# Kernel tuning notes

Hardware: AMD Instinct MI355X
Metric: run time of the kernel (lower is better)

Reference implementation:

```python
import jax, jax.numpy as jnp
import numpy as np

N_LABELS = 24
LABEL_DIM = 256
NEG = -10000.0


def setup_inputs() -> dict:
    key = jax.random.key(0)
    k1, k2 = jax.random.split(key, 2)
    B, L, DIM = 8, 512, 1024
    features = jax.random.normal(k1, (B, L, DIM), dtype=jnp.float32)
    mask = jnp.ones((B, L), dtype=bool)
    w_ff = jax.random.normal(k2, (N_LABELS * LABEL_DIM * 2, DIM), dtype=jnp.float32) * 0.02
    b_ff = jnp.zeros((N_LABELS * LABEL_DIM * 2,), dtype=jnp.float32)
    bias = jnp.zeros((N_LABELS,), dtype=jnp.float32)
    return {"features": features, "mask": mask, "w_ff": w_ff, "b_ff": b_ff, "bias": bias}


def reference(features, mask, w_ff, b_ff, bias):
    B, L, _ = features.shape
    # ff -> relu -> split into start/end features per label
    x = jax.nn.relu(jnp.einsum('bld,od->blo', features, w_ff) + b_ff)  # [B,L,n_labels*label_dim*2]
    x = x.reshape(B, L, N_LABELS, LABEL_DIM, 2)
    start_f = x[..., 0]  # [B,L,n_labels,label_dim]
    end_f = x[..., 1]
    # biaffine pairwise span scores: [B, n_labels, start, end]
    scores = jnp.einsum('bsld,beld->blse', start_f, end_f) + bias[None, :, None, None]
    # remove_nan branch: replace inf/nan with -10000
    scores = jnp.where(jnp.isinf(scores) | jnp.isnan(scores), NEG, scores)
    # triangular + padding mask over (start, end)
    triu = jnp.triu(jnp.ones((L, L), dtype=bool))  # start <= end
    spans_mask = triu[None] & mask[:, :, None] & mask[:, None, :]  # [B,L,L]
    masked_scores = jnp.where(spans_mask[:, None, :, :], scores, NEG)
    return scores, masked_scores
```

## Files before the change

### kernel.cpp

```cpp
#include <hip/hip_runtime.h>
#include <hip/hip_bf16.h>

#define NLAB  24
#define LDIM  256
#define LSEQ  512
#define DDIM  1024
#define NOUT  12288
#define NEGV  (-10000.0f)
#define MOFF  50331648L

typedef __attribute__((ext_vector_type(8))) short short8;
typedef __attribute__((ext_vector_type(4))) float f32x4;
typedef unsigned short u16;
typedef unsigned int   u32;

typedef const __attribute__((address_space(1))) void gvoid_t;
typedef __attribute__((address_space(3))) void lvoid_t;

__device__ __forceinline__ u16 f2bf(float f) {
  u32 u = __builtin_bit_cast(u32, f);
  u32 r = u + 0x7FFFu + ((u >> 16) & 1u);
  return (u16)(r >> 16);
}

__device__ __forceinline__ void g2l16(const u16* g, u16* l) {
  __builtin_amdgcn_global_load_lds((gvoid_t*)g, (lvoid_t*)l, 16, 0, 0);
}

__global__ void cvt_bf16_kernel(const float* __restrict__ feat,
                                const float* __restrict__ wff,
                                u16* __restrict__ fA, u16* __restrict__ fB) {
  const long NA = 4194304L;
  const long NB = 12582912L;
  const long NQ = (NA + NB) / 4;
  long stride = (long)gridDim.x * blockDim.x;
  for (long i = (long)blockIdx.x * blockDim.x + threadIdx.x; i < NQ; i += stride) {
    long e = i * 4;
    const float* s; u16* d;
    if (e < NA) { s = feat + e;        d = fA + e; }
    else        { s = wff + (e - NA);  d = fB + (e - NA); }
    float4 v = *reinterpret_cast<const float4*>(s);
    ushort4 o;
    o.x = f2bf(v.x); o.y = f2bf(v.y); o.z = f2bf(v.z); o.w = f2bf(v.w);
    *reinterpret_cast<ushort4*>(d) = o;
  }
}

template<int LDK, bool PERM>
__device__ __forceinline__ void stage_tile(const u16* __restrict__ gbase, int row0,
                                           int k0, u16* lbuf, int t) {
#pragma unroll
  for (int l = 0; l < 4; ++l) {
    const int rt = l * 64 + (t >> 3);
    const int ce = ((t & 7) ^ (rt & 7)) << 3;
    int gr = rt;
    if (PERM) gr = (rt & ~31) | ((rt & 15) << 1) | ((rt >> 4) & 1);
    g2l16(gbase + (long)(row0 + gr) * LDK + k0 + ce, lbuf + (l * 512 + t) * 8);
  }
}

#define FRAG_OFF(r, ks, hi) (((r) * 64 + (ks) * 32 + (hi) * 8) ^ (((r) & 7) << 3))

__global__ __launch_bounds__(512, 2)
void ff_gemm256(const u16* __restrict__ A, const u16* __restrict__ B,
                const float* __restrict__ bff,
                u16* __restrict__ sf, u16* __restrict__ ef) {
  __shared__ __align__(16) u16 lds[2][2][16384];
  const int tid = threadIdx.x, lane = tid & 63, wv = tid >> 6;
  const int wm = wv >> 2, wn = wv & 3;
  const int lr = lane & 15, hi = lane >> 4;

  const int bid = blockIdx.x;
  const int wg  = (bid & 7) * 96 + (bid >> 3);
  const int tm  = wg & 15, tn = wg >> 4;
  const int rowA0 = tm * 256, rowB0 = tn * 256;

  f32x4 acc[8][4] = {};

  stage_tile<DDIM, false>(A, rowA0, 0, lds[0][0], tid);
  stage_tile<DDIM, true >(B, rowB0, 0, lds[0][1], tid);
  __syncthreads();

  int buf = 0;
  for (int t = 0; t < 16; ++t) {
    if (t < 15) {
      stage_tile<DDIM, false>(A, rowA0, (t + 1) * 64, lds[buf ^ 1][0], tid);
      stage_tile<DDIM, true >(B, rowB0, (t + 1) * 64, lds[buf ^ 1][1], tid);
    }
    const u16* La = lds[buf][0];
    const u16* Lb = lds[buf][1];
#pragma unroll
    for (int ks = 0; ks < 2; ++ks) {
      short8 af[8], bfr[4];
#pragma unroll
      for (int i = 0; i < 8; ++i) {
        const int r = wm * 128 + i * 16 + lr;
        af[i] = *reinterpret_cast<const short8*>(La + FRAG_OFF(r, ks, hi));
      }
#pragma unroll
      for (int j = 0; j < 4; ++j) {
        const int r = wn * 64 + j * 16 + lr;
        bfr[j] = *reinterpret_cast<const short8*>(Lb + FRAG_OFF(r, ks, hi));
      }
      __builtin_amdgcn_s_setprio(1);
#pragma unroll
      for (int i = 0; i < 8; ++i)
#pragma unroll
        for (int j = 0; j < 4; ++j)
          acc[i][j] = __builtin_amdgcn_mfma_f32_16x16x32_bf16(af[i], bfr[j], acc[i][j], 0, 0, 0);
      __builtin_amdgcn_s_setprio(0);
    }
    __syncthreads();
    buf ^= 1;
  }

#pragma unroll
  for (int j = 0; j < 4; ++j) {
    const int cblk = wn * 64 + j * 16;
    const int o = rowB0 + (cblk & ~31) + 2 * lr + ((cblk >> 4) & 1);
    const float bv = bff[o];
    const int label = o >> 9, d = (o >> 1) & 255, se = o & 1;
    u16* dst = se ? ef : sf;
#pragma unroll
    for (int i = 0; i < 8; ++i) {
#pragma unroll
      for (int r = 0; r < 4; ++r) {
        const int m = rowA0 + wm * 128 + i * 16 + hi * 4 + r;
        const int b = m >> 9, ll = m & 511;
        float v = acc[i][j][r] + bv;
        v = v > 0.f ? v : 0.f;
        dst[((long)(b * NLAB + label) * LSEQ + ll) * LDIM + d] = f2bf(v);
      }
    }
  }
}

__global__ __launch_bounds__(512, 2)
void biaffine256(const u16* __restrict__ sf, const u16* __restrict__ ef,
                 const float* __restrict__ bias, const int* __restrict__ mask,
                 float* __restrict__ out) {
  __shared__ __align__(16) u16 lds[2][2][16384];
  const int tid = threadIdx.x, lane = tid & 63, wv = tid >> 6;
  const int wm = wv >> 2, wn = wv & 3;
  const int lr = lane & 15, hi = lane >> 4;

  const int bid = blockIdx.x;
  const int wg  = (bid & 7) * 96 + (bid >> 3);
  const int bl  = wg >> 2, tile = wg & 3;
  const int tm  = tile >> 1, tn = tile & 1;
  const int b = bl / NLAB, label = bl - b * NLAB;
  const u16* Ab = sf + (long)bl * LSEQ * LDIM;
  const u16* Bb = ef + (long)bl * LSEQ * LDIM;
  const int rowA0 = tm * 256, rowB0 = tn * 256;

  f32x4 acc[8][4] = {};

  stage_tile<LDIM, false>(Ab, rowA0, 0, lds[0][0], tid);
  stage_tile<LDIM, false>(Bb, rowB0, 0, lds[0][1], tid);
  __syncthreads();

  int buf = 0;
  for (int t = 0; t < 4; ++t) {
    if (t < 3) {
      stage_tile<LDIM, false>(Ab, rowA0, (t + 1) * 64, lds[buf ^ 1][0], tid);
      stage_tile<LDIM, false>(Bb, rowB0, (t + 1) * 64, lds[buf ^ 1][1], tid);
    }
    const u16* La = lds[buf][0];
    const u16* Lb = lds[buf][1];
#pragma unroll
    for (int ks = 0; ks < 2; ++ks) {
      short8 af[8], bfr[4];
#pragma unroll
      for (int i = 0; i < 8; ++i) {
        const int r = wm * 128 + i * 16 + lr;
        af[i] = *reinterpret_cast<const short8*>(La + FRAG_OFF(r, ks, hi));
      }
#pragma unroll
      for (int j = 0; j < 4; ++j) {
        const int r = wn * 64 + j * 16 + lr;
        bfr[j] = *reinterpret_cast<const short8*>(Lb + FRAG_OFF(r, ks, hi));
      }
      __builtin_amdgcn_s_setprio(1);
#pragma unroll
      for (int i = 0; i < 8; ++i)
#pragma unroll
        for (int j = 0; j < 4; ++j)
          acc[i][j] = __builtin_amdgcn_mfma_f32_16x16x32_bf16(af[i], bfr[j], acc[i][j], 0, 0, 0);
      __builtin_amdgcn_s_setprio(0);
    }
    __syncthreads();
    buf ^= 1;
  }

  const float bv = bias[label];
  const long obase = (long)bl * LSEQ * LSEQ;
#pragma unroll
  for (int i = 0; i < 8; ++i) {
#pragma unroll
    for (int r = 0; r < 4; ++r) {
      const int s = rowA0 + wm * 128 + i * 16 + hi * 4 + r;
      const bool ms = (mask[b * LSEQ + s] != 0);
      const long rbase = obase + (long)s * LSEQ;
#pragma unroll
      for (int j = 0; j < 4; ++j) {
        const int e = rowB0 + wn * 64 + j * 16 + lr;
        float v = acc[i][j][r] + bv;
        u32 bits = __builtin_bit_cast(u32, v);
        if ((bits & 0x7F800000u) == 0x7F800000u) v = NEGV;
        out[rbase + e] = v;
        const bool keep = (s <= e) && ms && (mask[b * LSEQ + e] != 0);
        out[MOFF + rbase + e] = keep ? v : NEGV;
      }
    }
  }
}

extern "C" void kernel_launch(void* const* d_in, const int* in_sizes, int n_in,
                              void* d_out, int out_size, void* d_ws, size_t ws_size,
                              hipStream_t stream) {
  const float* feat = (const float*)d_in[0];
  const int*   mask = (const int*)d_in[1];
  const float* wff  = (const float*)d_in[2];
  const float* bff  = (const float*)d_in[3];
  const float* bias = (const float*)d_in[4];
  float* out = (float*)d_out;

  u16* fA = (u16*)d_ws;
  u16* fB = fA + 4194304L;
  u16* sf = fB + 12582912L;
  u16* ef = sf + 25165824L;

  cvt_bf16_kernel<<<2048, 256, 0, stream>>>(feat, wff, fA, fB);
  ff_gemm256<<<768, 512, 0, stream>>>(fA, fB, bff, sf, ef);
  biaffine256<<<768, 512, 0, stream>>>(sf, ef, bias, mask, out);
}
```

Before: 254.0 us.

## Interleave async tile loads with MFMA phases in ff GEMM main loop

Replaces the simple double-buffered loop in the feed-forward GEMM with a hand-scheduled pipeline. Each K-step is split into eight phases that interleave partial global-to-LDS loads, LDS fragment reads and half-sized MFMA groups, with explicit s_barrier, vmcnt and lgkmcnt waits and sched_barriers. Global load addresses are precomputed once per thread. The goal is to hide memory latency behind matrix math and avoid full __syncthreads stalls, at the cost of fragile manual synchronisation and more barriers per iteration.

```diff
diff --git a/kernel.cpp b/kernel.cpp
--- a/kernel.cpp
+++ b/kernel.cpp
@@ -61,6 +61,33 @@
 
 #define FRAG_OFF(r, ks, hi) (((r) * 64 + (ks) * 32 + (hi) * 8) ^ (((r) & 7) << 3))
 
+
+#define SA_(P,H,KT) do { _Pragma("unroll") for (int l = 2*(H); l < 2*(H)+2; ++l) \
+    g2l16(gA[l] + (KT) * 64, &lds[P][0][ldst[l]]); } while (0)
+#define SBW(P,H,KT) do { _Pragma("unroll") for (int l = 2*(H); l < 2*(H)+2; ++l) \
+    g2l16(gB[l] + (KT) * 64, &lds[P][1][ldst[l]]); } while (0)
+#define RD_(P,KS) do { \
+    _Pragma("unroll") for (int i = 0; i < 8; ++i) { const int r = wm * 128 + i * 16 + lr; \
+      af[i] = *reinterpret_cast<const short8*>(&lds[P][0][FRAG_OFF(r, KS, hi)]); } \
+    _Pragma("unroll") for (int j = 0; j < 4; ++j) { const int r = wn * 64 + j * 16 + lr; \
+      bfr[j] = *reinterpret_cast<const short8*>(&lds[P][1][FRAG_OFF(r, KS, hi)]); } \
+  } while (0)
+#define MQ_(AFP,IB) do { \
+    _Pragma("unroll") for (int ii = 0; ii < 4; ++ii) \
+      _Pragma("unroll") for (int j = 0; j < 4; ++j) \
+        acc[(IB)+ii][j] = __builtin_amdgcn_mfma_f32_16x16x32_bf16((AFP)[ii], bfr[j], acc[(IB)+ii][j], 0, 0, 0); \
+  } while (0)
+#define SB0_() __builtin_amdgcn_sched_barrier(0)
+#define BARR_() __builtin_amdgcn_s_barrier()
+#define LGKM0_() asm volatile("s_waitcnt lgkmcnt(0)" ::: "memory")
+#define VM2_() asm volatile("s_waitcnt vmcnt(2)" ::: "memory")
+#define VM0_() asm volatile("s_waitcnt vmcnt(0)" ::: "memory")
+#define PH_MFMA(AFP,IB) do { \
+    SB0_(); BARR_(); LGKM0_(); SB0_(); \
+    __builtin_amdgcn_s_setprio(1); MQ_(AFP, IB); __builtin_amdgcn_s_setprio(0); \
+    SB0_(); BARR_(); \
+  } while (0)
+
 __global__ __launch_bounds__(512, 2)
 void ff_gemm256(const u16* __restrict__ A, const u16* __restrict__ B,
                 const float* __restrict__ bff,
@@ -75,43 +102,38 @@
   const int tm  = wg & 15, tn = wg >> 4;
   const int rowA0 = tm * 256, rowB0 = tn * 256;
 
+  const u16* gA[4]; const u16* gB[4]; int ldst[4];
+#pragma unroll
+  for (int l = 0; l < 4; ++l) {
+    const int rt = l * 64 + (tid >> 3);
+    const int ce = ((tid & 7) ^ (rt & 7)) << 3;
+    gA[l] = A + (long)(rowA0 + rt) * DDIM + ce;
+    const int gr = (rt & ~31) | ((rt & 15) << 1) | ((rt >> 4) & 1);
+    gB[l] = B + (long)(rowB0 + gr) * DDIM + ce;
+    ldst[l] = (l * 512 + tid) * 8;
+  }
+
   f32x4 acc[8][4] = {};
-
-  stage_tile<DDIM, false>(A, rowA0, 0, lds[0][0], tid);
-  stage_tile<DDIM, true >(B, rowB0, 0, lds[0][1], tid);
-  __syncthreads();
-
-  int buf = 0;
-  for (int t = 0; t < 16; ++t) {
-    if (t < 15) {
-      stage_tile<DDIM, false>(A, rowA0, (t + 1) * 64, lds[buf ^ 1][0], tid);
-      stage_tile<DDIM, true >(B, rowB0, (t + 1) * 64, lds[buf ^ 1][1], tid);
-    }
-    const u16* La = lds[buf][0];
-    const u16* Lb = lds[buf][1];
-#pragma unroll
-    for (int ks = 0; ks < 2; ++ks) {
-      short8 af[8], bfr[4];
-#pragma unroll
-      for (int i = 0; i < 8; ++i) {
-        const int r = wm * 128 + i * 16 + lr;
-        af[i] = *reinterpret_cast<const short8*>(La + FRAG_OFF(r, ks, hi));
-      }
-#pragma unroll
-      for (int j = 0; j < 4; ++j) {
-        const int r = wn * 64 + j * 16 + lr;
-        bfr[j] = *reinterpret_cast<const short8*>(Lb + FRAG_OFF(r, ks, hi));
-      }
-      __builtin_amdgcn_s_setprio(1);
-#pragma unroll
-      for (int i = 0; i < 8; ++i)
-#pragma unroll
-        for (int j = 0; j < 4; ++j)
-          acc[i][j] = __builtin_amdgcn_mfma_f32_16x16x32_bf16(af[i], bfr[j], acc[i][j], 0, 0, 0);
-      __builtin_amdgcn_s_setprio(0);
-    }
-    __syncthreads();
-    buf ^= 1;
+  short8 af[8], bfr[4];
+
+  SA_(0, 0, 0); SA_(0, 1, 0); SBW(0, 0, 0); SBW(0, 1, 0);
+  SA_(1, 0, 1);
+  SB0_(); VM2_(); BARR_();
+
+#pragma unroll 1
+  for (int t = 0; t < 8; ++t) {
+    const int o = 2 * t + 1, e2 = 2 * t + 2, o2 = 2 * t + 3;
+    const bool more = (t < 7);
+      RD_(0, 0); SA_(1, 1, o);                 PH_MFMA(af, 0);
+      SBW(1, 0, o);                            PH_MFMA(af + 4, 4);
+      RD_(0, 1); SBW(1, 1, o);                 PH_MFMA(af, 0);
+      if (more) { SA_(0, 0, e2); SB0_(); VM2_(); } else { SB0_(); VM0_(); }
+                                                        PH_MFMA(af + 4, 4);
+      RD_(1, 0); if (more) SA_(0, 1, e2);      PH_MFMA(af, 0);
+      if (more) SBW(0, 0, e2);                 PH_MFMA(af + 4, 4);
+      RD_(1, 1); if (more) SBW(0, 1, e2);      PH_MFMA(af, 0);
+      if (more) { SA_(1, 0, o2); SB0_(); VM2_(); }
+                                                        PH_MFMA(af + 4, 4);
   }
 
 #pragma unroll
```

After: 383.0 us. 1.51x slower.

## Triple-buffer FF GEMM K-loop with K=32 stages and manual waitcnt barriers

Applied to the files above, without the earlier changes.

Rewrites the feed-forward GEMM main loop as a 3-slot LDS ring with 32-wide K steps, keeping two tiles in flight. It replaces __syncthreads with explicit vmcnt/lgkmcnt waits plus s_barrier, so global-to-LDS loads overlap MFMA work. Fragment offsets and global pointers are precomputed with a new 4-chunk XOR swizzle to cut address math. The loop now runs 32 iterations, with one barrier per 32 MFMAs instead of per 64, which raises synchronisation overhead. LDS use drops, which could help occupancy.

```diff
diff --git a/kernel.cpp b/kernel.cpp
--- a/kernel.cpp
+++ b/kernel.cpp
@@ -46,6 +46,107 @@
   }
 }
 
+__global__ __launch_bounds__(512, 2)
+void ff_gemm256(const u16* __restrict__ A, const u16* __restrict__ B,
+                const float* __restrict__ bff,
+                u16* __restrict__ sf, u16* __restrict__ ef) {
+  __shared__ __align__(16) u16 lds[3][2][8192];
+  const int tid = threadIdx.x, lane = tid & 63, wv = tid >> 6;
+  const int wm = wv >> 2, wn = wv & 3;
+  const int lr = lane & 15, hi = lane >> 4;
+
+  const int bid = blockIdx.x;
+  const int wg  = (bid & 7) * 96 + (bid >> 3);
+  const int tm  = wg & 15, tn = wg >> 4;
+  const int rowA0 = tm * 256, rowB0 = tn * 256;
+
+  const u16* gAa[2]; const u16* gBa[2]; int dsta[2];
+#pragma unroll
+  for (int L = 0; L < 2; ++L) {
+    const int g = L * 512 + tid;
+    const int r = g >> 2;
+    const int c = (g & 3) ^ ((g >> 3) & 3);
+    gAa[L] = A + (long)(rowA0 + r) * DDIM + c * 8;
+    const int gr = (r & ~31) | ((r & 15) << 1) | ((r >> 4) & 1);
+    gBa[L] = B + (long)(rowB0 + gr) * DDIM + c * 8;
+    dsta[L] = g * 8;
+  }
+
+  int offA[8], offB[4];
+#pragma unroll
+  for (int i = 0; i < 8; ++i) { const int r = wm * 128 + i * 16 + lr; offA[i] = (4 * r + (hi ^ ((r >> 1) & 3))) * 8; }
+#pragma unroll
+  for (int j = 0; j < 4; ++j) { const int r = wn * 64 + j * 16 + lr; offB[j] = (4 * r + (hi ^ ((r >> 1) & 3))) * 8; }
+
+  f32x4 acc[8][4] = {};
+
+#pragma unroll
+  for (int L = 0; L < 2; ++L) g2l16(gAa[L],      &lds[0][0][dsta[L]]);
+#pragma unroll
+  for (int L = 0; L < 2; ++L) g2l16(gBa[L],      &lds[0][1][dsta[L]]);
+#pragma unroll
+  for (int L = 0; L < 2; ++L) g2l16(gAa[L] + 32, &lds[1][0][dsta[L]]);
+#pragma unroll
+  for (int L = 0; L < 2; ++L) g2l16(gBa[L] + 32, &lds[1][1][dsta[L]]);
+  __builtin_amdgcn_sched_barrier(0);
+  asm volatile("s_waitcnt vmcnt(4)" ::: "memory");
+  __builtin_amdgcn_s_barrier();
+
+  int slot = 0;
+#pragma unroll 1
+  for (int t = 0; t < 32; ++t) {
+    const u16* La = lds[slot][0];
+    const u16* Lb = lds[slot][1];
+    short8 af[8], bfr[4];
+#pragma unroll
+    for (int i = 0; i < 8; ++i) af[i] = *reinterpret_cast<const short8*>(La + offA[i]);
+#pragma unroll
+    for (int j = 0; j < 4; ++j) bfr[j] = *reinterpret_cast<const short8*>(Lb + offB[j]);
+    if (t < 30) {
+      int ns = slot + 2; if (ns >= 3) ns -= 3;
+      const int ko = (t + 2) * 32;
+#pragma unroll
+      for (int L = 0; L < 2; ++L) g2l16(gAa[L] + ko, &lds[ns][0][dsta[L]]);
+#pragma unroll
+      for (int L = 0; L < 2; ++L) g2l16(gBa[L] + ko, &lds[ns][1][dsta[L]]);
+    }
+    asm volatile("s_waitcnt lgkmcnt(0)" ::: "memory");
+    __builtin_amdgcn_sched_barrier(0);
+    __builtin_amdgcn_s_setprio(1);
+#pragma unroll
+    for (int i = 0; i < 8; ++i)
+#pragma unroll
+      for (int j = 0; j < 4; ++j)
+        acc[i][j] = __builtin_amdgcn_mfma_f32_16x16x32_bf16(af[i], bfr[j], acc[i][j], 0, 0, 0);
+    __builtin_amdgcn_s_setprio(0);
+    __builtin_amdgcn_sched_barrier(0);
+    if (t < 30)       asm volatile("s_waitcnt vmcnt(4)" ::: "memory");
+    else if (t == 30) asm volatile("s_waitcnt vmcnt(0)" ::: "memory");
+    __builtin_amdgcn_s_barrier();
+    slot += 1; if (slot >= 3) slot -= 3;
+  }
+
+#pragma unroll
+  for (int j = 0; j < 4; ++j) {
+    const int cblk = wn * 64 + j * 16;
+    const int o = rowB0 + (cblk & ~31) + 2 * lr + ((cblk >> 4) & 1);
+    const float bv = bff[o];
+    const int label = o >> 9, d = (o >> 1) & 255, se = o & 1;
+    u16* dst = se ? ef : sf;
+#pragma unroll
+    for (int i = 0; i < 8; ++i) {
+#pragma unroll
+      for (int r = 0; r < 4; ++r) {
+        const int m = rowA0 + wm * 128 + i * 16 + hi * 4 + r;
+        const int b = m >> 9, ll = m & 511;
+        float v = acc[i][j][r] + bv;
+        v = v > 0.f ? v : 0.f;
+        dst[((long)(b * NLAB + label) * LSEQ + ll) * LDIM + d] = f2bf(v);
+      }
+    }
+  }
+}
+
 template<int LDK, bool PERM>
 __device__ __forceinline__ void stage_tile(const u16* __restrict__ gbase, int row0,
                                            int k0, u16* lbuf, int t) {
@@ -60,80 +161,6 @@
 }
 
 #define FRAG_OFF(r, ks, hi) (((r) * 64 + (ks) * 32 + (hi) * 8) ^ (((r) & 7) << 3))
-
-__global__ __launch_bounds__(512, 2)
-void ff_gemm256(const u16* __restrict__ A, const u16* __restrict__ B,
-                const float* __restrict__ bff,
-                u16* __restrict__ sf, u16* __restrict__ ef) {
-  __shared__ __align__(16) u16 lds[2][2][16384];
-  const int tid = threadIdx.x, lane = tid & 63, wv = tid >> 6;
-  const int wm = wv >> 2, wn = wv & 3;
-  const int lr = lane & 15, hi = lane >> 4;
-
-  const int bid = blockIdx.x;
-  const int wg  = (bid & 7) * 96 + (bid >> 3);
-  const int tm  = wg & 15, tn = wg >> 4;
-  const int rowA0 = tm * 256, rowB0 = tn * 256;
-
-  f32x4 acc[8][4] = {};
-
-  stage_tile<DDIM, false>(A, rowA0, 0, lds[0][0], tid);
-  stage_tile<DDIM, true >(B, rowB0, 0, lds[0][1], tid);
-  __syncthreads();
-
-  int buf = 0;
-  for (int t = 0; t < 16; ++t) {
-    if (t < 15) {
-      stage_tile<DDIM, false>(A, rowA0, (t + 1) * 64, lds[buf ^ 1][0], tid);
-      stage_tile<DDIM, true >(B, rowB0, (t + 1) * 64, lds[buf ^ 1][1], tid);
-    }
-    const u16* La = lds[buf][0];
-    const u16* Lb = lds[buf][1];
-#pragma unroll
-    for (int ks = 0; ks < 2; ++ks) {
-      short8 af[8], bfr[4];
-#pragma unroll
-      for (int i = 0; i < 8; ++i) {
-        const int r = wm * 128 + i * 16 + lr;
-        af[i] = *reinterpret_cast<const short8*>(La + FRAG_OFF(r, ks, hi));
-      }
-#pragma unroll
-      for (int j = 0; j < 4; ++j) {
-        const int r = wn * 64 + j * 16 + lr;
-        bfr[j] = *reinterpret_cast<const short8*>(Lb + FRAG_OFF(r, ks, hi));
-      }
-      __builtin_amdgcn_s_setprio(1);
-#pragma unroll
-      for (int i = 0; i < 8; ++i)
-#pragma unroll
-        for (int j = 0; j < 4; ++j)
-          acc[i][j] = __builtin_amdgcn_mfma_f32_16x16x32_bf16(af[i], bfr[j], acc[i][j], 0, 0, 0);
-      __builtin_amdgcn_s_setprio(0);
-    }
-    __syncthreads();
-    buf ^= 1;
-  }
-
-#pragma unroll
-  for (int j = 0; j < 4; ++j) {
-    const int cblk = wn * 64 + j * 16;
-    const int o = rowB0 + (cblk & ~31) + 2 * lr + ((cblk >> 4) & 1);
-    const float bv = bff[o];
-    const int label = o >> 9, d = (o >> 1) & 255, se = o & 1;
-    u16* dst = se ? ef : sf;
-#pragma unroll
-    for (int i = 0; i < 8; ++i) {
-#pragma unroll
-      for (int r = 0; r < 4; ++r) {
-        const int m = rowA0 + wm * 128 + i * 16 + hi * 4 + r;
-        const int b = m >> 9, ll = m & 511;
-        float v = acc[i][j][r] + bv;
-        v = v > 0.f ? v : 0.f;
-        dst[((long)(b * NLAB + label) * LSEQ + ll) * LDIM + d] = f2bf(v);
-      }
-    }
-  }
-}
 
 __global__ __launch_bounds__(512, 2)
 void biaffine256(const u16* __restrict__ sf, const u16* __restrict__ ef,
```

After: 260.4 us. 1.02x slower.

## Shrink biaffine tiles to 128x128 with 256-thread blocks and K=32 steps

Applied to the files above, without the earlier changes.

Rewrites the biaffine kernel to use 128x128 output tiles computed by 4 waves, with 3072 blocks instead of 768 and a K step of 32 over 8 iterations. LDS addresses are precomputed with a new swizzle, and the end-position mask is hoisted out of the inner store loop. The aim is more blocks and more occupancy per CU, so that the store-heavy epilogue overlaps better with other blocks' compute. In exchange, operand tiles are re-read from global memory more often, and each iteration does less work between barriers.

```diff
diff --git a/kernel.cpp b/kernel.cpp
--- a/kernel.cpp
+++ b/kernel.cpp
@@ -135,70 +135,87 @@
   }
 }
 
-__global__ __launch_bounds__(512, 2)
-void biaffine256(const u16* __restrict__ sf, const u16* __restrict__ ef,
+#define RD_OFF(r, hi) ((4 * (r) + ((hi) ^ (((r) >> 1) & 3))) * 8)
+
+__global__ __launch_bounds__(256, 4)
+void biaffine128(const u16* __restrict__ sf, const u16* __restrict__ ef,
                  const float* __restrict__ bias, const int* __restrict__ mask,
                  float* __restrict__ out) {
-  __shared__ __align__(16) u16 lds[2][2][16384];
+  __shared__ __align__(16) u16 lds[2][2][4096];
   const int tid = threadIdx.x, lane = tid & 63, wv = tid >> 6;
-  const int wm = wv >> 2, wn = wv & 3;
+  const int wm = wv >> 1, wn = wv & 1;
   const int lr = lane & 15, hi = lane >> 4;
 
   const int bid = blockIdx.x;
-  const int wg  = (bid & 7) * 96 + (bid >> 3);
-  const int bl  = wg >> 2, tile = wg & 3;
-  const int tm  = tile >> 1, tn = tile & 1;
+  const int wg  = (bid & 7) * 384 + (bid >> 3);
+  const int bl  = wg >> 4, tile = wg & 15;
+  const int tm  = tile >> 2, tn = tile & 3;
   const int b = bl / NLAB, label = bl - b * NLAB;
   const u16* Ab = sf + (long)bl * LSEQ * LDIM;
   const u16* Bb = ef + (long)bl * LSEQ * LDIM;
-  const int rowA0 = tm * 256, rowB0 = tn * 256;
-
-  f32x4 acc[8][4] = {};
-
-  stage_tile<LDIM, false>(Ab, rowA0, 0, lds[0][0], tid);
-  stage_tile<LDIM, false>(Bb, rowB0, 0, lds[0][1], tid);
+  const int rowA0 = tm * 128, rowB0 = tn * 128;
+
+  const u16* gAa[2]; const u16* gBa[2]; int dsta[2];
+#pragma unroll
+  for (int L = 0; L < 2; ++L) {
+    const int g = L * 256 + tid;
+    const int r = g >> 2;
+    const int c = (g & 3) ^ ((g >> 3) & 3);
+    gAa[L] = Ab + (long)(rowA0 + r) * LDIM + c * 8;
+    gBa[L] = Bb + (long)(rowB0 + r) * LDIM + c * 8;
+    dsta[L] = g * 8;
+  }
+
+  int offA[4], offB[4];
+#pragma unroll
+  for (int i = 0; i < 4; ++i) { offA[i] = RD_OFF(wm * 64 + i * 16 + lr, hi); }
+#pragma unroll
+  for (int j = 0; j < 4; ++j) { offB[j] = RD_OFF(wn * 64 + j * 16 + lr, hi); }
+
+  f32x4 acc[4][4] = {};
+
+#pragma unroll
+  for (int L = 0; L < 2; ++L) g2l16(gAa[L], &lds[0][0][dsta[L]]);
+#pragma unroll
+  for (int L = 0; L < 2; ++L) g2l16(gBa[L], &lds[0][1][dsta[L]]);
   __syncthreads();
 
-  int buf = 0;
-  for (int t = 0; t < 4; ++t) {
-    if (t < 3) {
-      stage_tile<LDIM, false>(Ab, rowA0, (t + 1) * 64, lds[buf ^ 1][0], tid);
-      stage_tile<LDIM, false>(Bb, rowB0, (t + 1) * 64, lds[buf ^ 1][1], tid);
-    }
-    const u16* La = lds[buf][0];
-    const u16* Lb = lds[buf][1];
-#pragma unroll
-    for (int ks = 0; ks < 2; ++ks) {
-      short8 af[8], bfr[4];
-#pragma unroll
-      for (int i = 0; i < 8; ++i) {
-        const int r = wm * 128 + i * 16 + lr;
-        af[i] = *reinterpret_cast<const short8*>(La + FRAG_OFF(r, ks, hi));
-      }
-#pragma unroll
-      for (int j = 0; j < 4; ++j) {
-        const int r = wn * 64 + j * 16 + lr;
-        bfr[j] = *reinterpret_cast<const short8*>(Lb + FRAG_OFF(r, ks, hi));
-      }
-      __builtin_amdgcn_s_setprio(1);
-#pragma unroll
-      for (int i = 0; i < 8; ++i)
-#pragma unroll
-        for (int j = 0; j < 4; ++j)
-          acc[i][j] = __builtin_amdgcn_mfma_f32_16x16x32_bf16(af[i], bfr[j], acc[i][j], 0, 0, 0);
-      __builtin_amdgcn_s_setprio(0);
-    }
+#pragma unroll 1
+  for (int t = 0; t < 8; ++t) {
+    if (t < 7) {
+      const int ko = (t + 1) * 32, nb = (t + 1) & 1;
+#pragma unroll
+      for (int L = 0; L < 2; ++L) g2l16(gAa[L] + ko, &lds[nb][0][dsta[L]]);
+#pragma unroll
+      for (int L = 0; L < 2; ++L) g2l16(gBa[L] + ko, &lds[nb][1][dsta[L]]);
+    }
+    const u16* La = lds[t & 1][0];
+    const u16* Lb = lds[t & 1][1];
+    short8 af[4], bfr[4];
+#pragma unroll
+    for (int i = 0; i < 4; ++i) af[i] = *reinterpret_cast<const short8*>(La + offA[i]);
+#pragma unroll
+    for (int j = 0; j < 4; ++j) bfr[j] = *reinterpret_cast<const short8*>(Lb + offB[j]);
+    __builtin_amdgcn_s_setprio(1);
+#pragma unroll
+    for (int i = 0; i < 4; ++i)
+#pragma unroll
+      for (int j = 0; j < 4; ++j)
+        acc[i][j] = __builtin_amdgcn_mfma_f32_16x16x32_bf16(af[i], bfr[j], acc[i][j], 0, 0, 0);
+    __builtin_amdgcn_s_setprio(0);
     __syncthreads();
-    buf ^= 1;
   }
 
   const float bv = bias[label];
   const long obase = (long)bl * LSEQ * LSEQ;
-#pragma unroll
-  for (int i = 0; i < 8; ++i) {
+  bool me[4];
+#pragma unroll
+  for (int j = 0; j < 4; ++j) me[j] = (mask[b * LSEQ + rowB0 + wn * 64 + j * 16 + lr] != 0);
+#pragma unroll
+  for (int i = 0; i < 4; ++i) {
 #pragma unroll
     for (int r = 0; r < 4; ++r) {
-      const int s = rowA0 + wm * 128 + i * 16 + hi * 4 + r;
+      const int s = rowA0 + wm * 64 + i * 16 + hi * 4 + r;
       const bool ms = (mask[b * LSEQ + s] != 0);
       const long rbase = obase + (long)s * LSEQ;
 #pragma unroll
@@ -208,7 +225,7 @@
         u32 bits = __builtin_bit_cast(u32, v);
         if ((bits & 0x7F800000u) == 0x7F800000u) v = NEGV;
         out[rbase + e] = v;
-        const bool keep = (s <= e) && ms && (mask[b * LSEQ + e] != 0);
+        const bool keep = (s <= e) && ms && me[j];
         out[MOFF + rbase + e] = keep ? v : NEGV;
       }
     }
@@ -232,5 +249,5 @@
 
   cvt_bf16_kernel<<<2048, 256, 0, stream>>>(feat, wff, fA, fB);
   ff_gemm256<<<768, 512, 0, stream>>>(fA, fB, bff, sf, ef);
-  biaffine256<<<768, 512, 0, stream>>>(sf, ef, bias, mask, out);
-}
+  biaffine128<<<3072, 256, 0, stream>>>(sf, ef, bias, mask, out);
+}
```

New measurement: 258.9 us. Within noise of the previous version (+1.9%).
